# Optimization experiments

Measured on AMD Instinct MI355X. Metric: run time of the kernel, lower is better.

Reference implementation:

```python
import jax, jax.numpy as jnp
import numpy as np

WINDOWS = (5, 10, 20)
EPS = 1e-4
K_SLICES = 3
OVERLAP = 0.5


def setup_inputs() -> dict:
    key = jax.random.key(0)
    k1, k2, k3, k4 = jax.random.split(key, 4)
    B, T, H = 64, 2048, 256
    x = jax.random.normal(k1, (B, T, H), dtype=jnp.float32)
    alpha = 0.1 * jax.random.normal(k2, (H, len(WINDOWS)), dtype=jnp.float32)
    gamma = 1.0 + 0.1 * jax.random.normal(k3, (K_SLICES, H), dtype=jnp.float32)
    beta = 0.1 * jax.random.normal(k4, (K_SLICES, H), dtype=jnp.float32)
    return {"x": x, "alpha": alpha, "gamma": gamma, "beta": beta}


def _fan(x, alpha):
    # FrequencyAdaptiveNormSimple: multi-window sliding mean/std, blended by softmax(alpha).
    B, T, H = x.shape
    al = jax.nn.softmax(alpha, axis=-1)  # [H, nW]
    # prefix sums for O(T) sliding statistics (same math as unfold mean/std)
    zrow = jnp.zeros((B, 1, H), x.dtype)
    S1 = jnp.concatenate([zrow, jnp.cumsum(x, axis=1)], axis=1)        # [B, T+1, H]
    S2 = jnp.concatenate([zrow, jnp.cumsum(x * x, axis=1)], axis=1)    # [B, T+1, H]
    out = jnp.zeros_like(x)
    for wi, w in enumerate(WINDOWS):
        if w > T:
            continue
        ws = S1[:, w:, :] - S1[:, : T - w + 1, :]    # window sums, [B, T-w+1, H]
        ws2 = S2[:, w:, :] - S2[:, : T - w + 1, :]
        mu = ws / w
        var = jnp.maximum((ws2 - ws * ws / w) / (w - 1), 0.0)  # unbiased (torch std default)
        sd = jnp.maximum(jnp.sqrt(var), EPS)
        # F.pad(..., (w-1, 0), mode='replicate') on the time dim
        mu = jnp.pad(mu, ((0, 0), (w - 1, 0), (0, 0)), mode="edge")
        sd = jnp.pad(sd, ((0, 0), (w - 1, 0), (0, 0)), mode="edge")
        z = jnp.nan_to_num((x - mu) / sd, nan=0.0, posinf=0.0, neginf=0.0)
        out = out + z * al[:, wi][None, None, :]
    return out


def _san(x, gamma, beta):
    # SliceAdaptiveNormSimple: overlapping slices, per-slice (B,T) stats (detached), affine, avg.
    B, T, H = x.shape
    step = max(1, int(round(T / (K_SLICES - (K_SLICES - 1) * OVERLAP))))
    win = min(T, step + int(round(step * OVERLAP)))
    y = jnp.zeros_like(x)
    cnt = jnp.zeros((B, T, 1), x.dtype)
    s = 0
    for k in range(K_SLICES):
        e = min(T, s + win)
        if e <= s:
            break
        xk = x[:, s:e, :]
        mu = jax.lax.stop_gradient(jnp.mean(xk, axis=(0, 1), keepdims=True))
        sd = jax.lax.stop_gradient(
            jnp.maximum(jnp.std(xk, axis=(0, 1), ddof=1, keepdims=True), 1e-4)
        )
        z = jnp.nan_to_num((xk - mu) / sd, nan=0.0, posinf=0.0, neginf=0.0)
        z = z * gamma[k][None, None, :] + beta[k][None, None, :]
        y = y.at[:, s:e, :].add(z)
        cnt = cnt.at[:, s:e, :].add(1.0)
        s += step
    return y / (cnt + EPS)


def reference(x, alpha, gamma, beta):
    # StableFANSAN: out = x + SAN(FAN(x))
    return x + _san(_fan(x, alpha), gamma, beta)
```

## Files before the change

kernel.cpp:

```cpp
#include <hip/hip_runtime.h>

#define T_DIM 2048
#define H_DIM 256
#define B_DIM 64
#define CHUNK 128
#define NCH (T_DIM / CHUNK)
#define NCB (B_DIM * NCH)
#define EPS_F 1e-4f

__device__ __forceinline__ void win_stats(float s1, float s2, float inv_w, float inv_wm1,
                                          float& mu, float& isd) {
    mu = s1 * inv_w;
    float var = fmaxf((s2 - s1 * s1 * inv_w) * inv_wm1, 0.0f);
    isd = fminf(rsqrtf(var), 1e4f);
}

template <int PASS>
__global__ __launch_bounds__(256)
void fan_kernel(const float* __restrict__ x, const float* __restrict__ alpha,
                const float* __restrict__ gamma, const float* __restrict__ beta,
                float* __restrict__ part, const float* __restrict__ acc,
                float* __restrict__ out) {
    const int blk = blockIdx.x;
    const int b = blk / NCH;
    const int c = blk % NCH;
    const int h = threadIdx.x;
    const int t0 = c * CHUNK;
    const float* xbh = x + (size_t)b * T_DIM * H_DIM + h;

    const float a0 = alpha[h * 3 + 0], a1 = alpha[h * 3 + 1], a2 = alpha[h * 3 + 2];
    const float mx = fmaxf(a0, fmaxf(a1, a2));
    const float e0 = __expf(a0 - mx), e1 = __expf(a1 - mx), e2 = __expf(a2 - mx);
    const float einv = 1.0f / (e0 + e1 + e2);
    const float al0 = e0 * einv, al1 = e1 * einv, al2 = e2 * einv;

    float mu0 = 0.f, isd0 = 0.f, g0 = 0.f, be0 = 0.f;
    float mu1 = 0.f, isd1 = 0.f, g1 = 0.f, be1 = 0.f;
    if (PASS == 1) {
        const float N0 = 64.0f * 1536.0f, N1 = 64.0f * 1024.0f;
        float S10 = acc[0 * H_DIM + h], S20 = acc[1 * H_DIM + h];
        float S11 = acc[2 * H_DIM + h], S21 = acc[3 * H_DIM + h];
        mu0 = S10 / N0;
        float v0 = fmaxf((S20 - S10 * S10 / N0) / (N0 - 1.0f), 0.0f);
        isd0 = 1.0f / fmaxf(sqrtf(v0), EPS_F);
        mu1 = S11 / N1;
        float v1 = fmaxf((S21 - S11 * S11 / N1) / (N1 - 1.0f), 0.0f);
        isd1 = 1.0f / fmaxf(sqrtf(v1), EPS_F);
        g0 = gamma[0 * H_DIM + h]; be0 = beta[0 * H_DIM + h];
        g1 = gamma[1 * H_DIM + h]; be1 = beta[1 * H_DIM + h];
    }

    float s1_5 = 0.f, s2_5 = 0.f, s1_10 = 0.f, s2_10 = 0.f, s1_20 = 0.f, s2_20 = 0.f;
    float mu5i = 0.f, isd5i = 0.f, mu10i = 0.f, isd10i = 0.f, mu20i = 0.f, isd20i = 0.f;
    const bool first = (c == 0);

    float hist[32];

    if (first) {
        float c1 = 0.f, c2 = 0.f;
#pragma unroll
        for (int j = 0; j < 20; ++j) {
            float v = xbh[j * H_DIM];
            c1 += v; c2 += v * v;
            if (j == 4)  win_stats(c1, c2, 0.2f,  0.25f,        mu5i,  isd5i);
            if (j == 9)  win_stats(c1, c2, 0.1f,  1.f / 9.f,    mu10i, isd10i);
            if (j == 19) win_stats(c1, c2, 0.05f, 1.f / 19.f,   mu20i, isd20i);
        }
#pragma unroll
        for (int j = 0; j < 32; ++j) hist[j] = 0.0f;
    } else {
#pragma unroll
        for (int j = 1; j <= 20; ++j) {
            float v = xbh[(t0 - j) * H_DIM];
            hist[(32 - j) & 31] = v;
            s1_20 += v; s2_20 += v * v;
            if (j <= 10) { s1_10 += v; s2_10 += v * v; }
            if (j <= 5)  { s1_5  += v; s2_5  += v * v; }
        }
#pragma unroll
        for (int j = 0; j < 12; ++j) hist[j] = 0.0f;
    }

    float ls1 = 0.0f, ls2 = 0.0f;

    for (int i0 = 0; i0 < CHUNK; i0 += 32) {
#pragma unroll
        for (int k = 0; k < 32; ++k) {
            const int t = t0 + i0 + k;
            const float v = xbh[t * H_DIM];
            hist[k] = v;
            s1_5  += v; s2_5  += v * v;
            s1_10 += v; s2_10 += v * v;
            s1_20 += v; s2_20 += v * v;
            if (!first || t >= 5)  { float o = hist[(k - 5)  & 31]; s1_5  -= o; s2_5  -= o * o; }
            if (!first || t >= 10) { float o = hist[(k - 10) & 31]; s1_10 -= o; s2_10 -= o * o; }
            if (!first || t >= 20) { float o = hist[(k - 20) & 31]; s1_20 -= o; s2_20 -= o * o; }

            float mu, isd, fan = 0.0f;
            if (!first || t >= 4)  win_stats(s1_5,  s2_5,  0.2f,  0.25f,      mu, isd);
            else { mu = mu5i;  isd = isd5i; }
            fan += (v - mu) * isd * al0;
            if (!first || t >= 9)  win_stats(s1_10, s2_10, 0.1f,  1.f / 9.f,  mu, isd);
            else { mu = mu10i; isd = isd10i; }
            fan += (v - mu) * isd * al1;
            if (!first || t >= 19) win_stats(s1_20, s2_20, 0.05f, 1.f / 19.f, mu, isd);
            else { mu = mu20i; isd = isd20i; }
            fan += (v - mu) * isd * al2;

            if (PASS == 0) {
                ls1 += fan; ls2 += fan * fan;
            } else {
                float z0 = (fan - mu0) * isd0 * g0 + be0;
                float z1 = (fan - mu1) * isd1 * g1 + be1;
                float y;
                if (t < 1024)       y = z0 * (1.0f / 1.0001f);
                else if (t >= 1536) y = z1 * (1.0f / 1.0001f);
                else                y = (z0 + z1) * (1.0f / 2.0001f);
                out[(size_t)(b * T_DIM + t) * H_DIM + h] = v + y;
            }
        }
    }

    if (PASS == 0) {
        const bool in0 = (c < 12), in1 = (c >= 8);
        part[(0 * NCB + blk) * H_DIM + h] = in0 ? ls1 : 0.0f;
        part[(1 * NCB + blk) * H_DIM + h] = in0 ? ls2 : 0.0f;
        part[(2 * NCB + blk) * H_DIM + h] = in1 ? ls1 : 0.0f;
        part[(3 * NCB + blk) * H_DIM + h] = in1 ? ls2 : 0.0f;
    }
}

__global__ __launch_bounds__(256)
void reduce_kernel(const float* __restrict__ part, float* __restrict__ acc) {
    const int h = threadIdx.x;
    const int k = blockIdx.x >> 4;
    const int g = blockIdx.x & 15;
    float a1 = 0.f, a2 = 0.f;
    for (int i = 0; i < NCB / 16; ++i) {
        const int cb = g * (NCB / 16) + i;
        a1 += part[((2 * k)     * NCB + cb) * H_DIM + h];
        a2 += part[((2 * k + 1) * NCB + cb) * H_DIM + h];
    }
    atomicAdd(&acc[(2 * k)     * H_DIM + h], a1);
    atomicAdd(&acc[(2 * k + 1) * H_DIM + h], a2);
}

extern "C" void kernel_launch(void* const* d_in, const int* in_sizes, int n_in,
                              void* d_out, int out_size, void* d_ws, size_t ws_size,
                              hipStream_t stream) {
    const float* x     = (const float*)d_in[0];
    const float* alpha = (const float*)d_in[1];
    const float* gamma = (const float*)d_in[2];
    const float* beta  = (const float*)d_in[3];
    float* out  = (float*)d_out;
    float* part = (float*)d_ws;
    float* acc  = part + 4 * NCB * H_DIM;

    hipMemsetAsync(acc, 0, 4 * H_DIM * sizeof(float), stream);
    fan_kernel<0><<<NCB, H_DIM, 0, stream>>>(x, alpha, gamma, beta, part, acc, out);
    reduce_kernel<<<32, H_DIM, 0, stream>>>(part, acc);
    fan_kernel<1><<<NCB, H_DIM, 0, stream>>>(x, alpha, gamma, beta, part, acc, out);
}
```

Baseline: 386.9 us.

## Halve chunk size, specialize first chunk, fold SAN affine into per-chunk FMA

Chunk length drops from 128 to 64, doubling the block count so more waves can hide memory latency. The price is more halo re-reads (20 extra rows per chunk) and a larger partial buffer. The first chunk gets its own templated path, which removes runtime boundary branches from the inner loop. The per-slice normalization and averaging are folded into one precomputed scale and offset per chunk, so each output is a single FMA. Pass 0 now writes only two partial arrays, and slice membership moves into the reduce kernel; launch bounds also request 6 blocks per CU.

```diff
diff --git a/kernel.cpp b/kernel.cpp
--- a/kernel.cpp
+++ b/kernel.cpp
@@ -3,7 +3,7 @@
 #define T_DIM 2048
 #define H_DIM 256
 #define B_DIM 64
-#define CHUNK 128
+#define CHUNK 64
 #define NCH (T_DIM / CHUNK)
 #define NCB (B_DIM * NCH)
 #define EPS_F 1e-4f
@@ -15,57 +15,17 @@
     isd = fminf(rsqrtf(var), 1e4f);
 }
 
-template <int PASS>
-__global__ __launch_bounds__(256)
-void fan_kernel(const float* __restrict__ x, const float* __restrict__ alpha,
-                const float* __restrict__ gamma, const float* __restrict__ beta,
-                float* __restrict__ part, const float* __restrict__ acc,
-                float* __restrict__ out) {
-    const int blk = blockIdx.x;
-    const int b = blk / NCH;
-    const int c = blk % NCH;
-    const int h = threadIdx.x;
-    const int t0 = c * CHUNK;
-    const float* xbh = x + (size_t)b * T_DIM * H_DIM + h;
-
-    const float a0 = alpha[h * 3 + 0], a1 = alpha[h * 3 + 1], a2 = alpha[h * 3 + 2];
-    const float mx = fmaxf(a0, fmaxf(a1, a2));
-    const float e0 = __expf(a0 - mx), e1 = __expf(a1 - mx), e2 = __expf(a2 - mx);
-    const float einv = 1.0f / (e0 + e1 + e2);
-    const float al0 = e0 * einv, al1 = e1 * einv, al2 = e2 * einv;
-
-    float mu0 = 0.f, isd0 = 0.f, g0 = 0.f, be0 = 0.f;
-    float mu1 = 0.f, isd1 = 0.f, g1 = 0.f, be1 = 0.f;
-    if (PASS == 1) {
-        const float N0 = 64.0f * 1536.0f, N1 = 64.0f * 1024.0f;
-        float S10 = acc[0 * H_DIM + h], S20 = acc[1 * H_DIM + h];
-        float S11 = acc[2 * H_DIM + h], S21 = acc[3 * H_DIM + h];
-        mu0 = S10 / N0;
-        float v0 = fmaxf((S20 - S10 * S10 / N0) / (N0 - 1.0f), 0.0f);
-        isd0 = 1.0f / fmaxf(sqrtf(v0), EPS_F);
-        mu1 = S11 / N1;
-        float v1 = fmaxf((S21 - S11 * S11 / N1) / (N1 - 1.0f), 0.0f);
-        isd1 = 1.0f / fmaxf(sqrtf(v1), EPS_F);
-        g0 = gamma[0 * H_DIM + h]; be0 = beta[0 * H_DIM + h];
-        g1 = gamma[1 * H_DIM + h]; be1 = beta[1 * H_DIM + h];
-    }
+template <int PASS, bool FIRST>
+__device__ __forceinline__ void run_chunk(
+    const float* __restrict__ xbh, int t0, float al0, float al1, float al2,
+    float A, float Bc, float* __restrict__ outbh,
+    float& ls1, float& ls2,
+    float mu5i, float isd5i, float mu10i, float isd10i, float mu20i, float isd20i) {
 
     float s1_5 = 0.f, s2_5 = 0.f, s1_10 = 0.f, s2_10 = 0.f, s1_20 = 0.f, s2_20 = 0.f;
-    float mu5i = 0.f, isd5i = 0.f, mu10i = 0.f, isd10i = 0.f, mu20i = 0.f, isd20i = 0.f;
-    const bool first = (c == 0);
-
     float hist[32];
 
-    if (first) {
-        float c1 = 0.f, c2 = 0.f;
-#pragma unroll
-        for (int j = 0; j < 20; ++j) {
-            float v = xbh[j * H_DIM];
-            c1 += v; c2 += v * v;
-            if (j == 4)  win_stats(c1, c2, 0.2f,  0.25f,        mu5i,  isd5i);
-            if (j == 9)  win_stats(c1, c2, 0.1f,  1.f / 9.f,    mu10i, isd10i);
-            if (j == 19) win_stats(c1, c2, 0.05f, 1.f / 19.f,   mu20i, isd20i);
-        }
+    if (FIRST) {
 #pragma unroll
         for (int j = 0; j < 32; ++j) hist[j] = 0.0f;
     } else {
@@ -77,11 +37,7 @@
             if (j <= 10) { s1_10 += v; s2_10 += v * v; }
             if (j <= 5)  { s1_5  += v; s2_5  += v * v; }
         }
-#pragma unroll
-        for (int j = 0; j < 12; ++j) hist[j] = 0.0f;
     }
-
-    float ls1 = 0.0f, ls2 = 0.0f;
 
     for (int i0 = 0; i0 < CHUNK; i0 += 32) {
 #pragma unroll
@@ -92,41 +48,92 @@
             s1_5  += v; s2_5  += v * v;
             s1_10 += v; s2_10 += v * v;
             s1_20 += v; s2_20 += v * v;
-            if (!first || t >= 5)  { float o = hist[(k - 5)  & 31]; s1_5  -= o; s2_5  -= o * o; }
-            if (!first || t >= 10) { float o = hist[(k - 10) & 31]; s1_10 -= o; s2_10 -= o * o; }
-            if (!first || t >= 20) { float o = hist[(k - 20) & 31]; s1_20 -= o; s2_20 -= o * o; }
+            if (!FIRST || i0 + k >= 5)  { float o = hist[(k - 5)  & 31]; s1_5  -= o; s2_5  -= o * o; }
+            if (!FIRST || i0 + k >= 10) { float o = hist[(k - 10) & 31]; s1_10 -= o; s2_10 -= o * o; }
+            if (!FIRST || i0 + k >= 20) { float o = hist[(k - 20) & 31]; s1_20 -= o; s2_20 -= o * o; }
 
             float mu, isd, fan = 0.0f;
-            if (!first || t >= 4)  win_stats(s1_5,  s2_5,  0.2f,  0.25f,      mu, isd);
+            if (!FIRST || i0 + k >= 4)  win_stats(s1_5,  s2_5,  0.2f,  0.25f,      mu, isd);
             else { mu = mu5i;  isd = isd5i; }
             fan += (v - mu) * isd * al0;
-            if (!first || t >= 9)  win_stats(s1_10, s2_10, 0.1f,  1.f / 9.f,  mu, isd);
+            if (!FIRST || i0 + k >= 9)  win_stats(s1_10, s2_10, 0.1f,  1.f / 9.f,  mu, isd);
             else { mu = mu10i; isd = isd10i; }
             fan += (v - mu) * isd * al1;
-            if (!first || t >= 19) win_stats(s1_20, s2_20, 0.05f, 1.f / 19.f, mu, isd);
+            if (!FIRST || i0 + k >= 19) win_stats(s1_20, s2_20, 0.05f, 1.f / 19.f, mu, isd);
             else { mu = mu20i; isd = isd20i; }
             fan += (v - mu) * isd * al2;
 
             if (PASS == 0) {
                 ls1 += fan; ls2 += fan * fan;
             } else {
-                float z0 = (fan - mu0) * isd0 * g0 + be0;
-                float z1 = (fan - mu1) * isd1 * g1 + be1;
-                float y;
-                if (t < 1024)       y = z0 * (1.0f / 1.0001f);
-                else if (t >= 1536) y = z1 * (1.0f / 1.0001f);
-                else                y = (z0 + z1) * (1.0f / 2.0001f);
-                out[(size_t)(b * T_DIM + t) * H_DIM + h] = v + y;
+                outbh[t * H_DIM] = v + fmaf(fan, A, Bc);
             }
         }
     }
+}
+
+template <int PASS>
+__global__ __launch_bounds__(256, 6)
+void fan_kernel(const float* __restrict__ x, const float* __restrict__ alpha,
+                const float* __restrict__ gamma, const float* __restrict__ beta,
+                float* __restrict__ part, const float* __restrict__ acc,
+                float* __restrict__ out) {
+    const int blk = blockIdx.x;
+    const int b = blk / NCH;
+    const int c = blk % NCH;
+    const int h = threadIdx.x;
+    const int t0 = c * CHUNK;
+    const float* xbh = x + (size_t)b * T_DIM * H_DIM + h;
+    float* outbh = out + (size_t)b * T_DIM * H_DIM + h;
+
+    const float a0 = alpha[h * 3 + 0], a1 = alpha[h * 3 + 1], a2 = alpha[h * 3 + 2];
+    const float mx = fmaxf(a0, fmaxf(a1, a2));
+    const float e0 = __expf(a0 - mx), e1 = __expf(a1 - mx), e2 = __expf(a2 - mx);
+    const float einv = 1.0f / (e0 + e1 + e2);
+    const float al0 = e0 * einv, al1 = e1 * einv, al2 = e2 * einv;
+
+    float A = 0.f, Bc = 0.f;
+    if (PASS == 1) {
+        const float N0 = 64.0f * 1536.0f, N1 = 64.0f * 1024.0f;
+        float S10 = acc[0 * H_DIM + h], S20 = acc[1 * H_DIM + h];
+        float S11 = acc[2 * H_DIM + h], S21 = acc[3 * H_DIM + h];
+        float mu0 = S10 / N0;
+        float v0 = fmaxf((S20 - S10 * S10 / N0) / (N0 - 1.0f), 0.0f);
+        float isd0 = 1.0f / fmaxf(sqrtf(v0), EPS_F);
+        float mu1 = S11 / N1;
+        float v1 = fmaxf((S21 - S11 * S11 / N1) / (N1 - 1.0f), 0.0f);
+        float isd1 = 1.0f / fmaxf(sqrtf(v1), EPS_F);
+        float A0 = isd0 * gamma[0 * H_DIM + h], B0 = beta[0 * H_DIM + h] - mu0 * A0;
+        float A1 = isd1 * gamma[1 * H_DIM + h], B1 = beta[1 * H_DIM + h] - mu1 * A1;
+        const float r1 = 1.0f / 1.0001f, r2 = 1.0f / 2.0001f;
+        if (c < 16)      { A = A0 * r1;        Bc = B0 * r1; }
+        else if (c >= 24){ A = A1 * r1;        Bc = B1 * r1; }
+        else             { A = (A0 + A1) * r2; Bc = (B0 + B1) * r2; }
+    }
+
+    float ls1 = 0.0f, ls2 = 0.0f;
+
+    if (c == 0) {
+        float mu5i, isd5i, mu10i, isd10i, mu20i, isd20i;
+        float c1 = 0.f, c2 = 0.f;
+#pragma unroll
+        for (int j = 0; j < 20; ++j) {
+            float v = xbh[j * H_DIM];
+            c1 += v; c2 += v * v;
+            if (j == 4)  win_stats(c1, c2, 0.2f,  0.25f,      mu5i,  isd5i);
+            if (j == 9)  win_stats(c1, c2, 0.1f,  1.f / 9.f,  mu10i, isd10i);
+            if (j == 19) win_stats(c1, c2, 0.05f, 1.f / 19.f, mu20i, isd20i);
+        }
+        run_chunk<PASS, true>(xbh, t0, al0, al1, al2, A, Bc, outbh, ls1, ls2,
+                              mu5i, isd5i, mu10i, isd10i, mu20i, isd20i);
+    } else {
+        run_chunk<PASS, false>(xbh, t0, al0, al1, al2, A, Bc, outbh, ls1, ls2,
+                               0.f, 0.f, 0.f, 0.f, 0.f, 0.f);
+    }
 
     if (PASS == 0) {
-        const bool in0 = (c < 12), in1 = (c >= 8);
-        part[(0 * NCB + blk) * H_DIM + h] = in0 ? ls1 : 0.0f;
-        part[(1 * NCB + blk) * H_DIM + h] = in0 ? ls2 : 0.0f;
-        part[(2 * NCB + blk) * H_DIM + h] = in1 ? ls1 : 0.0f;
-        part[(3 * NCB + blk) * H_DIM + h] = in1 ? ls2 : 0.0f;
+        part[(0 * NCB + blk) * H_DIM + h] = ls1;
+        part[(1 * NCB + blk) * H_DIM + h] = ls2;
     }
 }
 
@@ -137,9 +144,13 @@
     const int g = blockIdx.x & 15;
     float a1 = 0.f, a2 = 0.f;
     for (int i = 0; i < NCB / 16; ++i) {
-        const int cb = g * (NCB / 16) + i;
-        a1 += part[((2 * k)     * NCB + cb) * H_DIM + h];
-        a2 += part[((2 * k + 1) * NCB + cb) * H_DIM + h];
+        const int blk = g * (NCB / 16) + i;
+        const int c = blk % NCH;
+        const bool member = (k == 0) ? (c < 24) : (c >= 16);
+        if (member) {
+            a1 += part[(0 * NCB + blk) * H_DIM + h];
+            a2 += part[(1 * NCB + blk) * H_DIM + h];
+        }
     }
     atomicAdd(&acc[(2 * k)     * H_DIM + h], a1);
     atomicAdd(&acc[(2 * k + 1) * H_DIM + h], a2);
@@ -154,7 +165,7 @@
     const float* beta  = (const float*)d_in[3];
     float* out  = (float*)d_out;
     float* part = (float*)d_ws;
-    float* acc  = part + 4 * NCB * H_DIM;
+    float* acc  = part + 2 * NCB * H_DIM;
 
     hipMemsetAsync(acc, 0, 4 * H_DIM * sizeof(float), stream);
     fan_kernel<0><<<NCB, H_DIM, 0, stream>>>(x, alpha, gamma, beta, part, acc, out);
```

Measured after the change: 745.2 us. +92.6%, slower.
